# Performance work log

Measured on AMD Instinct MI355X. Metric: run time of the kernel, lower is better.

## Reference

```python
import jax, jax.numpy as jnp
import numpy as np

# --- Instant-NGP hash grid hyperparameters ---
L = 12            # n_levels (multires)
T = 2 ** 19       # hash table size per level
F = 2             # features per level -> feature_dim = L*F = 24
BASE_RES = 16
MAX_RES = 2048
N_PTS = 524288
D_OUT = 257

_growth = np.exp((np.log(MAX_RES) - np.log(BASE_RES)) / (L - 1))
RES = np.floor(BASE_RES * _growth ** np.arange(L)).astype(np.int32)  # per-level grid resolution
PRIMES = jnp.array([1, 2654435761, 805459861], dtype=jnp.uint32)
# 8 corner offsets of a voxel, [8,3] in {0,1}
OFFS = np.array([[(i >> 2) & 1, (i >> 1) & 1, i & 1] for i in range(8)], dtype=np.int32)
OFFS_U32 = jnp.asarray(OFFS, dtype=jnp.uint32)
OFFS_BOOL = jnp.asarray(OFFS.astype(bool))


def hash_encode(x, tables):
    """x: [N,3] in [0,1]; tables: [L,T,F]. Returns [N, L*F]."""
    outs = []
    for l in range(L):
        pos = x * RES[l]                      # [N,3]
        p0 = jnp.floor(pos)
        frac = pos - p0                       # [N,3] trilinear fractions
        corners = p0.astype(jnp.uint32)[:, None, :] + OFFS_U32[None]  # [N,8,3]
        h = corners * PRIMES[None, None, :]   # uint32 wrap-around mult
        idx = (h[..., 0] ^ h[..., 1] ^ h[..., 2]) & jnp.uint32(T - 1)  # [N,8]
        feats = tables[l][idx.astype(jnp.int32)]                       # [N,8,F] gather
        # trilinear weights: prod over dims of frac or (1-frac)
        w = jnp.prod(jnp.where(OFFS_BOOL[None], frac[:, None, :], 1.0 - frac[:, None, :]), axis=-1)  # [N,8]
        # windowed_embed: coarse-to-fine window weight; alpha = L (fully trained) -> weight 1.0
        outs.append(jnp.einsum('nc,ncf->nf', w, feats))
    return jnp.concatenate(outs, axis=-1)     # [N, L*F]


def setup_inputs() -> dict:
    key = jax.random.key(0)
    k1, k2, k3 = jax.random.split(key, 3)
    inputs = jax.random.uniform(k1, (N_PTS, 3), dtype=jnp.float32)
    tables = jax.random.normal(k2, (L, T, F), dtype=jnp.float32) * 1e-2
    W = jax.random.normal(k3, (L * F, D_OUT), dtype=jnp.float32) * (1.0 / np.sqrt(L * F))
    bias = jnp.zeros((D_OUT,), dtype=jnp.float32)
    return {"inputs": inputs, "tables": tables, "W": W, "bias": bias}


def reference(inputs, tables, W, bias):
    emb = hash_encode(inputs, tables)          # [N, 24]
    y = emb @ W + bias                         # TCNNLinear head, [N, 257]
    # torch.cat([x[:, :1], x[:, 1:]], -1) is identity; keep for fidelity
    return jnp.concatenate([y[:, :1], y[:, 1:]], axis=-1)
```

## Files before the change

### kernel.cpp

```cpp
#include <hip/hip_runtime.h>
#include <math.h>

#define NLEV 12
#define TSIZE (1u << 19)
#define TMASK (TSIZE - 1u)
#define DOUT 257
#define PPB 256
#define EMB 24
#define RSTRIDE 28
#define TP 128

struct ResArr { float r[NLEV]; };

__global__ __launch_bounds__(256)
void encode_kernel(const float* __restrict__ xin,
                   const float* __restrict__ tables,
                   float2* __restrict__ emb2,
                   int N, ResArr res)
{
    const int p = blockIdx.x * 256 + threadIdx.x;
    if (p >= N) return;
    const float px = xin[3 * p + 0];
    const float py = xin[3 * p + 1];
    const float pz = xin[3 * p + 2];
#pragma unroll 2
    for (int l = 0; l < NLEV; ++l) {
        const float rf = res.r[l];
        const float sx = px * rf, sy = py * rf, sz = pz * rf;
        const float gx = floorf(sx), gy = floorf(sy), gz = floorf(sz);
        const float tx = sx - gx, ty = sy - gy, tz = sz - gz;
        const unsigned ix = (unsigned)gx, iy = (unsigned)gy, iz = (unsigned)gz;
        const unsigned hx0 = ix,               hx1 = ix + 1u;
        const unsigned hy0 = iy * 2654435761u, hy1 = hy0 + 2654435761u;
        const unsigned hz0 = iz * 805459861u,  hz1 = hz0 + 805459861u;
        const float2* __restrict__ tab = (const float2*)tables + (size_t)l * TSIZE;
        float2 f0 = tab[(hx0 ^ hy0 ^ hz0) & TMASK];
        float2 f1 = tab[(hx0 ^ hy0 ^ hz1) & TMASK];
        float2 f2 = tab[(hx0 ^ hy1 ^ hz0) & TMASK];
        float2 f3 = tab[(hx0 ^ hy1 ^ hz1) & TMASK];
        float2 f4 = tab[(hx1 ^ hy0 ^ hz0) & TMASK];
        float2 f5 = tab[(hx1 ^ hy0 ^ hz1) & TMASK];
        float2 f6 = tab[(hx1 ^ hy1 ^ hz0) & TMASK];
        float2 f7 = tab[(hx1 ^ hy1 ^ hz1) & TMASK];
        const float u0 = 1.0f - tx, u1 = tx;
        const float v0 = 1.0f - ty, v1 = ty;
        const float s0 = 1.0f - tz, s1 = tz;
        const float w0 = (u0 * v0) * s0;
        const float w1 = (u0 * v0) * s1;
        const float w2 = (u0 * v1) * s0;
        const float w3 = (u0 * v1) * s1;
        const float w4 = (u1 * v0) * s0;
        const float w5 = (u1 * v0) * s1;
        const float w6 = (u1 * v1) * s0;
        const float w7 = (u1 * v1) * s1;
        float a = w0 * f0.x;
        float b = w0 * f0.y;
        a = fmaf(w1, f1.x, a);  b = fmaf(w1, f1.y, b);
        a = fmaf(w2, f2.x, a);  b = fmaf(w2, f2.y, b);
        a = fmaf(w3, f3.x, a);  b = fmaf(w3, f3.y, b);
        a = fmaf(w4, f4.x, a);  b = fmaf(w4, f4.y, b);
        a = fmaf(w5, f5.x, a);  b = fmaf(w5, f5.y, b);
        a = fmaf(w6, f6.x, a);  b = fmaf(w6, f6.y, b);
        a = fmaf(w7, f7.x, a);  b = fmaf(w7, f7.y, b);
        emb2[(size_t)l * N + p] = make_float2(a, b);
    }
}

__global__ __launch_bounds__(256)
void head_kernel(const float2* __restrict__ emb2,
                 const float* __restrict__ Wm,
                 const float* __restrict__ bias,
                 float* __restrict__ out,
                 int N)
{
    __shared__ float2 sm[NLEV][TP];
    const int tid  = threadIdx.x;
    const int base = blockIdx.x * TP;
    const int nv   = min(TP, N - base);

    float wcol[EMB];
#pragma unroll
    for (int k = 0; k < EMB; ++k) wcol[k] = Wm[k * DOUT + tid];
    const float bj = bias[tid];

#pragma unroll
    for (int i = 0; i < (NLEV * TP) / 256; ++i) {
        const int f = i * 256 + tid;
        const int l = f >> 7;
        const int n = f & (TP - 1);
        if (n < nv) sm[l][n] = emb2[(size_t)l * N + base + n];
    }
    __syncthreads();

    float* orow = out + (size_t)base * DOUT + tid;
    for (int n = 0; n < nv; ++n, orow += DOUT) {
        float accA = bj, accB = 0.0f;
#pragma unroll
        for (int l = 0; l < NLEV; l += 2) {
            const float2 q0 = sm[l][n];
            const float2 q1 = sm[l + 1][n];
            accA = fmaf(q0.x, wcol[2 * l + 0], accA);
            accB = fmaf(q0.y, wcol[2 * l + 1], accB);
            accA = fmaf(q1.x, wcol[2 * l + 2], accA);
            accB = fmaf(q1.y, wcol[2 * l + 3], accB);
        }
        *orow = accA + accB;
    }

    if (tid < nv) {
        float acc = bias[256];
#pragma unroll
        for (int l = 0; l < NLEV; ++l) {
            const float2 q = sm[l][tid];
            acc = fmaf(q.x, Wm[(2 * l) * DOUT + 256],
                  fmaf(q.y, Wm[(2 * l + 1) * DOUT + 256], acc));
        }
        out[(size_t)(base + tid) * DOUT + 256] = acc;
    }
}

__global__ __launch_bounds__(256)
void hashgrid_head_kernel(const float* __restrict__ xin,
                          const float* __restrict__ tables,
                          const float* __restrict__ Wm,
                          const float* __restrict__ bias,
                          float* __restrict__ out,
                          int N, ResArr res)
{
    __shared__ float emb[PPB * RSTRIDE];
    const int tid  = threadIdx.x;
    const int base = blockIdx.x * PPB;
    const int p    = base + tid;

    float wcol[EMB];
#pragma unroll
    for (int k = 0; k < EMB; ++k) wcol[k] = Wm[k * DOUT + tid];
    const float bj = bias[tid];

    const bool extra = (tid < 64);
    float wext[EMB];
    float bext = 0.0f;
    if (extra) {
#pragma unroll
        for (int k = 0; k < EMB; ++k) wext[k] = Wm[k * DOUT + 256];
        bext = bias[256];
    }

    if (p < N) {
        const float px = xin[3 * p + 0];
        const float py = xin[3 * p + 1];
        const float pz = xin[3 * p + 2];
#pragma unroll 2
        for (int l = 0; l < NLEV; ++l) {
            const float rf = res.r[l];
            const float sx = px * rf, sy = py * rf, sz = pz * rf;
            const float gx = floorf(sx), gy = floorf(sy), gz = floorf(sz);
            const float tx = sx - gx, ty = sy - gy, tz = sz - gz;
            const unsigned ix = (unsigned)gx, iy = (unsigned)gy, iz = (unsigned)gz;
            const unsigned hx0 = ix,               hx1 = ix + 1u;
            const unsigned hy0 = iy * 2654435761u, hy1 = hy0 + 2654435761u;
            const unsigned hz0 = iz * 805459861u,  hz1 = hz0 + 805459861u;
            const float2* __restrict__ tab = (const float2*)tables + (size_t)l * TSIZE;
            float2 f0 = tab[(hx0 ^ hy0 ^ hz0) & TMASK];
            float2 f1 = tab[(hx0 ^ hy0 ^ hz1) & TMASK];
            float2 f2 = tab[(hx0 ^ hy1 ^ hz0) & TMASK];
            float2 f3 = tab[(hx0 ^ hy1 ^ hz1) & TMASK];
            float2 f4 = tab[(hx1 ^ hy0 ^ hz0) & TMASK];
            float2 f5 = tab[(hx1 ^ hy0 ^ hz1) & TMASK];
            float2 f6 = tab[(hx1 ^ hy1 ^ hz0) & TMASK];
            float2 f7 = tab[(hx1 ^ hy1 ^ hz1) & TMASK];
            const float u0 = 1.0f - tx, u1 = tx;
            const float v0 = 1.0f - ty, v1 = ty;
            const float s0 = 1.0f - tz, s1 = tz;
            const float w0 = (u0 * v0) * s0;
            const float w1 = (u0 * v0) * s1;
            const float w2 = (u0 * v1) * s0;
            const float w3 = (u0 * v1) * s1;
            const float w4 = (u1 * v0) * s0;
            const float w5 = (u1 * v0) * s1;
            const float w6 = (u1 * v1) * s0;
            const float w7 = (u1 * v1) * s1;
            float a = w0 * f0.x;
            float b = w0 * f0.y;
            a = fmaf(w1, f1.x, a);  b = fmaf(w1, f1.y, b);
            a = fmaf(w2, f2.x, a);  b = fmaf(w2, f2.y, b);
            a = fmaf(w3, f3.x, a);  b = fmaf(w3, f3.y, b);
            a = fmaf(w4, f4.x, a);  b = fmaf(w4, f4.y, b);
            a = fmaf(w5, f5.x, a);  b = fmaf(w5, f5.y, b);
            a = fmaf(w6, f6.x, a);  b = fmaf(w6, f6.y, b);
            a = fmaf(w7, f7.x, a);  b = fmaf(w7, f7.y, b);
            *(float2*)&emb[tid * RSTRIDE + 2 * l] = make_float2(a, b);
        }
    }

    __syncthreads();

    const int nvalid = min(PPB, N - base);
    for (int n = 0; n < nvalid; ++n) {
        const float4* e4 = (const float4*)&emb[n * RSTRIDE];
        float4 q0 = e4[0], q1 = e4[1], q2 = e4[2], q3 = e4[3], q4 = e4[4], q5 = e4[5];
        float e[EMB] = {q0.x, q0.y, q0.z, q0.w, q1.x, q1.y, q1.z, q1.w,
                        q2.x, q2.y, q2.z, q2.w, q3.x, q3.y, q3.z, q3.w,
                        q4.x, q4.y, q4.z, q4.w, q5.x, q5.y, q5.z, q5.w};
        float acc = bj;
#pragma unroll
        for (int k = 0; k < EMB; ++k) acc = fmaf(e[k], wcol[k], acc);
        out[(size_t)(base + n) * DOUT + tid] = acc;
        if (extra) {
            float acc2 = bext;
#pragma unroll
            for (int k = 0; k < EMB; ++k) acc2 = fmaf(e[k], wext[k], acc2);
            if (tid == 0) out[(size_t)(base + n) * DOUT + 256] = acc2;
        }
    }
}

extern "C" void kernel_launch(void* const* d_in, const int* in_sizes, int n_in,
                              void* d_out, int out_size, void* d_ws, size_t ws_size,
                              hipStream_t stream) {
    const float* xin    = (const float*)d_in[0];
    const float* tables = (const float*)d_in[1];
    const float* Wm     = (const float*)d_in[2];
    const float* bias   = (const float*)d_in[3];
    float* out = (float*)d_out;
    const int N = in_sizes[0] / 3;

    ResArr res;
    const double growth = exp((log(2048.0) - log(16.0)) / 11.0);
    for (int l = 0; l < NLEV; ++l)
        res.r[l] = (float)floor(16.0 * pow(growth, (double)l));

    const size_t need = (size_t)NLEV * (size_t)N * sizeof(float2);
    if (d_ws != nullptr && ws_size >= need) {
        float2* emb2 = (float2*)d_ws;
        hipLaunchKernelGGL(encode_kernel, dim3((N + 255) / 256), dim3(256), 0, stream,
                           xin, tables, emb2, N, res);
        hipLaunchKernelGGL(head_kernel, dim3((N + TP - 1) / TP), dim3(256), 0, stream,
                           emb2, Wm, bias, out, N);
    } else {
        const int grid = (N + PPB - 1) / PPB;
        hipLaunchKernelGGL(hashgrid_head_kernel, dim3(grid), dim3(PPB), 0, stream,
                           xin, tables, Wm, bias, out, N, res);
    }
}
```

Baseline: 917.0 us.

## Split hash encoding across levels per block and read embeddings directly in head

The encode kernel now launches one block per (level, point-chunk), so level-major block ordering keeps each level's hash table hot in cache and gives more parallel work. The head kernel drops its shared-memory staging and __syncthreads, reading embedding values straight from global memory with uniform (broadcast) loads per point. This trades repeated point-coordinate loads and redundant per-thread global reads for less cache thrashing and no LDS staging.

```diff
diff --git a/kernel.cpp b/kernel.cpp
--- a/kernel.cpp
+++ b/kernel.cpp
@@ -16,54 +16,55 @@
 void encode_kernel(const float* __restrict__ xin,
                    const float* __restrict__ tables,
                    float2* __restrict__ emb2,
-                   int N, ResArr res)
+                   int N, int nbpl, ResArr res)
 {
-    const int p = blockIdx.x * 256 + threadIdx.x;
+    const int lvl = blockIdx.x / nbpl;
+    const int bx  = blockIdx.x - lvl * nbpl;
+    const int p   = bx * 256 + threadIdx.x;
     if (p >= N) return;
+
     const float px = xin[3 * p + 0];
     const float py = xin[3 * p + 1];
     const float pz = xin[3 * p + 2];
-#pragma unroll 2
-    for (int l = 0; l < NLEV; ++l) {
-        const float rf = res.r[l];
-        const float sx = px * rf, sy = py * rf, sz = pz * rf;
-        const float gx = floorf(sx), gy = floorf(sy), gz = floorf(sz);
-        const float tx = sx - gx, ty = sy - gy, tz = sz - gz;
-        const unsigned ix = (unsigned)gx, iy = (unsigned)gy, iz = (unsigned)gz;
-        const unsigned hx0 = ix,               hx1 = ix + 1u;
-        const unsigned hy0 = iy * 2654435761u, hy1 = hy0 + 2654435761u;
-        const unsigned hz0 = iz * 805459861u,  hz1 = hz0 + 805459861u;
-        const float2* __restrict__ tab = (const float2*)tables + (size_t)l * TSIZE;
-        float2 f0 = tab[(hx0 ^ hy0 ^ hz0) & TMASK];
-        float2 f1 = tab[(hx0 ^ hy0 ^ hz1) & TMASK];
-        float2 f2 = tab[(hx0 ^ hy1 ^ hz0) & TMASK];
-        float2 f3 = tab[(hx0 ^ hy1 ^ hz1) & TMASK];
-        float2 f4 = tab[(hx1 ^ hy0 ^ hz0) & TMASK];
-        float2 f5 = tab[(hx1 ^ hy0 ^ hz1) & TMASK];
-        float2 f6 = tab[(hx1 ^ hy1 ^ hz0) & TMASK];
-        float2 f7 = tab[(hx1 ^ hy1 ^ hz1) & TMASK];
-        const float u0 = 1.0f - tx, u1 = tx;
-        const float v0 = 1.0f - ty, v1 = ty;
-        const float s0 = 1.0f - tz, s1 = tz;
-        const float w0 = (u0 * v0) * s0;
-        const float w1 = (u0 * v0) * s1;
-        const float w2 = (u0 * v1) * s0;
-        const float w3 = (u0 * v1) * s1;
-        const float w4 = (u1 * v0) * s0;
-        const float w5 = (u1 * v0) * s1;
-        const float w6 = (u1 * v1) * s0;
-        const float w7 = (u1 * v1) * s1;
-        float a = w0 * f0.x;
-        float b = w0 * f0.y;
-        a = fmaf(w1, f1.x, a);  b = fmaf(w1, f1.y, b);
-        a = fmaf(w2, f2.x, a);  b = fmaf(w2, f2.y, b);
-        a = fmaf(w3, f3.x, a);  b = fmaf(w3, f3.y, b);
-        a = fmaf(w4, f4.x, a);  b = fmaf(w4, f4.y, b);
-        a = fmaf(w5, f5.x, a);  b = fmaf(w5, f5.y, b);
-        a = fmaf(w6, f6.x, a);  b = fmaf(w6, f6.y, b);
-        a = fmaf(w7, f7.x, a);  b = fmaf(w7, f7.y, b);
-        emb2[(size_t)l * N + p] = make_float2(a, b);
-    }
+
+    const float rf = res.r[lvl];
+    const float sx = px * rf, sy = py * rf, sz = pz * rf;
+    const float gx = floorf(sx), gy = floorf(sy), gz = floorf(sz);
+    const float tx = sx - gx, ty = sy - gy, tz = sz - gz;
+    const unsigned ix = (unsigned)gx, iy = (unsigned)gy, iz = (unsigned)gz;
+    const unsigned hx0 = ix,               hx1 = ix + 1u;
+    const unsigned hy0 = iy * 2654435761u, hy1 = hy0 + 2654435761u;
+    const unsigned hz0 = iz * 805459861u,  hz1 = hz0 + 805459861u;
+    const float2* __restrict__ tab = (const float2*)tables + (size_t)lvl * TSIZE;
+    float2 f0 = tab[(hx0 ^ hy0 ^ hz0) & TMASK];
+    float2 f1 = tab[(hx0 ^ hy0 ^ hz1) & TMASK];
+    float2 f2 = tab[(hx0 ^ hy1 ^ hz0) & TMASK];
+    float2 f3 = tab[(hx0 ^ hy1 ^ hz1) & TMASK];
+    float2 f4 = tab[(hx1 ^ hy0 ^ hz0) & TMASK];
+    float2 f5 = tab[(hx1 ^ hy0 ^ hz1) & TMASK];
+    float2 f6 = tab[(hx1 ^ hy1 ^ hz0) & TMASK];
+    float2 f7 = tab[(hx1 ^ hy1 ^ hz1) & TMASK];
+    const float u0 = 1.0f - tx, u1 = tx;
+    const float v0 = 1.0f - ty, v1 = ty;
+    const float s0 = 1.0f - tz, s1 = tz;
+    const float w0 = (u0 * v0) * s0;
+    const float w1 = (u0 * v0) * s1;
+    const float w2 = (u0 * v1) * s0;
+    const float w3 = (u0 * v1) * s1;
+    const float w4 = (u1 * v0) * s0;
+    const float w5 = (u1 * v0) * s1;
+    const float w6 = (u1 * v1) * s0;
+    const float w7 = (u1 * v1) * s1;
+    float a = w0 * f0.x;
+    float b = w0 * f0.y;
+    a = fmaf(w1, f1.x, a);  b = fmaf(w1, f1.y, b);
+    a = fmaf(w2, f2.x, a);  b = fmaf(w2, f2.y, b);
+    a = fmaf(w3, f3.x, a);  b = fmaf(w3, f3.y, b);
+    a = fmaf(w4, f4.x, a);  b = fmaf(w4, f4.y, b);
+    a = fmaf(w5, f5.x, a);  b = fmaf(w5, f5.y, b);
+    a = fmaf(w6, f6.x, a);  b = fmaf(w6, f6.y, b);
+    a = fmaf(w7, f7.x, a);  b = fmaf(w7, f7.y, b);
+    emb2[(size_t)lvl * N + p] = make_float2(a, b);
 }
 
 __global__ __launch_bounds__(256)
@@ -73,7 +74,6 @@
                  float* __restrict__ out,
                  int N)
 {
-    __shared__ float2 sm[NLEV][TP];
     const int tid  = threadIdx.x;
     const int base = blockIdx.x * TP;
     const int nv   = min(TP, N - base);
@@ -83,39 +83,29 @@
     for (int k = 0; k < EMB; ++k) wcol[k] = Wm[k * DOUT + tid];
     const float bj = bias[tid];
 
-#pragma unroll
-    for (int i = 0; i < (NLEV * TP) / 256; ++i) {
-        const int f = i * 256 + tid;
-        const int l = f >> 7;
-        const int n = f & (TP - 1);
-        if (n < nv) sm[l][n] = emb2[(size_t)l * N + base + n];
-    }
-    __syncthreads();
-
     float* orow = out + (size_t)base * DOUT + tid;
+#pragma unroll 2
     for (int n = 0; n < nv; ++n, orow += DOUT) {
         float accA = bj, accB = 0.0f;
 #pragma unroll
-        for (int l = 0; l < NLEV; l += 2) {
-            const float2 q0 = sm[l][n];
-            const float2 q1 = sm[l + 1][n];
-            accA = fmaf(q0.x, wcol[2 * l + 0], accA);
-            accB = fmaf(q0.y, wcol[2 * l + 1], accB);
-            accA = fmaf(q1.x, wcol[2 * l + 2], accA);
-            accB = fmaf(q1.y, wcol[2 * l + 3], accB);
+        for (int l = 0; l < NLEV; ++l) {
+            const float2 q = emb2[(size_t)l * N + base + n];
+            accA = fmaf(q.x, wcol[2 * l + 0], accA);
+            accB = fmaf(q.y, wcol[2 * l + 1], accB);
         }
         *orow = accA + accB;
     }
 
     if (tid < nv) {
+        const int p = base + tid;
         float acc = bias[256];
 #pragma unroll
         for (int l = 0; l < NLEV; ++l) {
-            const float2 q = sm[l][tid];
+            const float2 q = emb2[(size_t)l * N + p];
             acc = fmaf(q.x, Wm[(2 * l) * DOUT + 256],
                   fmaf(q.y, Wm[(2 * l + 1) * DOUT + 256], acc));
         }
-        out[(size_t)(base + tid) * DOUT + 256] = acc;
+        out[(size_t)p * DOUT + 256] = acc;
     }
 }
 
@@ -233,8 +223,9 @@
     const size_t need = (size_t)NLEV * (size_t)N * sizeof(float2);
     if (d_ws != nullptr && ws_size >= need) {
         float2* emb2 = (float2*)d_ws;
-        hipLaunchKernelGGL(encode_kernel, dim3((N + 255) / 256), dim3(256), 0, stream,
-                           xin, tables, emb2, N, res);
+        const int nbpl = (N + 255) / 256;
+        hipLaunchKernelGGL(encode_kernel, dim3(nbpl * NLEV), dim3(256), 0, stream,
+                           xin, tables, emb2, N, nbpl, res);
         hipLaunchKernelGGL(head_kernel, dim3((N + TP - 1) / TP), dim3(256), 0, stream,
                            emb2, Wm, bias, out, N);
     } else {
```

After: 1.440 ms. 1.57x slower.

## Split hash encoding across levels in the grid for per-level table locality

Applied to the files above, without the earlier changes.

The encode kernel now assigns each block to a single hash level, with each thread handling two points, instead of one thread walking all twelve levels. Blocks that run at the same time then gather from the same 4 MB level table, which should improve L2 hit rates, and two independent gather sets per thread add memory-level parallelism. The cost is that point coordinates are reloaded once per level, and the fused fallback kernel is only refactored through a shared helper.

```diff
diff --git a/kernel.cpp b/kernel.cpp
--- a/kernel.cpp
+++ b/kernel.cpp
@@ -9,60 +9,98 @@
 #define EMB 24
 #define RSTRIDE 28
 #define TP 128
+#define EPT 2
+#define EPB (256 * EPT)
 
 struct ResArr { float r[NLEV]; };
+
+struct Corner { unsigned idx[8]; float w[8]; };
+
+__device__ __forceinline__ void hash_corners(float rf, float px, float py, float pz,
+                                             Corner& c)
+{
+    const float sx = px * rf, sy = py * rf, sz = pz * rf;
+    const float gx = floorf(sx), gy = floorf(sy), gz = floorf(sz);
+    const float tx = sx - gx, ty = sy - gy, tz = sz - gz;
+    const unsigned ix = (unsigned)gx, iy = (unsigned)gy, iz = (unsigned)gz;
+    const unsigned hx0 = ix,               hx1 = ix + 1u;
+    const unsigned hy0 = iy * 2654435761u, hy1 = hy0 + 2654435761u;
+    const unsigned hz0 = iz * 805459861u,  hz1 = hz0 + 805459861u;
+    c.idx[0] = (hx0 ^ hy0 ^ hz0) & TMASK;
+    c.idx[1] = (hx0 ^ hy0 ^ hz1) & TMASK;
+    c.idx[2] = (hx0 ^ hy1 ^ hz0) & TMASK;
+    c.idx[3] = (hx0 ^ hy1 ^ hz1) & TMASK;
+    c.idx[4] = (hx1 ^ hy0 ^ hz0) & TMASK;
+    c.idx[5] = (hx1 ^ hy0 ^ hz1) & TMASK;
+    c.idx[6] = (hx1 ^ hy1 ^ hz0) & TMASK;
+    c.idx[7] = (hx1 ^ hy1 ^ hz1) & TMASK;
+    const float u0 = 1.0f - tx, u1 = tx;
+    const float v0 = 1.0f - ty, v1 = ty;
+    const float s0 = 1.0f - tz, s1 = tz;
+    c.w[0] = (u0 * v0) * s0;
+    c.w[1] = (u0 * v0) * s1;
+    c.w[2] = (u0 * v1) * s0;
+    c.w[3] = (u0 * v1) * s1;
+    c.w[4] = (u1 * v0) * s0;
+    c.w[5] = (u1 * v0) * s1;
+    c.w[6] = (u1 * v1) * s0;
+    c.w[7] = (u1 * v1) * s1;
+}
 
 __global__ __launch_bounds__(256)
 void encode_kernel(const float* __restrict__ xin,
                    const float* __restrict__ tables,
                    float2* __restrict__ emb2,
-                   int N, ResArr res)
-{
-    const int p = blockIdx.x * 256 + threadIdx.x;
-    if (p >= N) return;
-    const float px = xin[3 * p + 0];
-    const float py = xin[3 * p + 1];
-    const float pz = xin[3 * p + 2];
-#pragma unroll 2
-    for (int l = 0; l < NLEV; ++l) {
-        const float rf = res.r[l];
-        const float sx = px * rf, sy = py * rf, sz = pz * rf;
-        const float gx = floorf(sx), gy = floorf(sy), gz = floorf(sz);
-        const float tx = sx - gx, ty = sy - gy, tz = sz - gz;
-        const unsigned ix = (unsigned)gx, iy = (unsigned)gy, iz = (unsigned)gz;
-        const unsigned hx0 = ix,               hx1 = ix + 1u;
-        const unsigned hy0 = iy * 2654435761u, hy1 = hy0 + 2654435761u;
-        const unsigned hz0 = iz * 805459861u,  hz1 = hz0 + 805459861u;
-        const float2* __restrict__ tab = (const float2*)tables + (size_t)l * TSIZE;
-        float2 f0 = tab[(hx0 ^ hy0 ^ hz0) & TMASK];
-        float2 f1 = tab[(hx0 ^ hy0 ^ hz1) & TMASK];
-        float2 f2 = tab[(hx0 ^ hy1 ^ hz0) & TMASK];
-        float2 f3 = tab[(hx0 ^ hy1 ^ hz1) & TMASK];
-        float2 f4 = tab[(hx1 ^ hy0 ^ hz0) & TMASK];
-        float2 f5 = tab[(hx1 ^ hy0 ^ hz1) & TMASK];
-        float2 f6 = tab[(hx1 ^ hy1 ^ hz0) & TMASK];
-        float2 f7 = tab[(hx1 ^ hy1 ^ hz1) & TMASK];
-        const float u0 = 1.0f - tx, u1 = tx;
-        const float v0 = 1.0f - ty, v1 = ty;
-        const float s0 = 1.0f - tz, s1 = tz;
-        const float w0 = (u0 * v0) * s0;
-        const float w1 = (u0 * v0) * s1;
-        const float w2 = (u0 * v1) * s0;
-        const float w3 = (u0 * v1) * s1;
-        const float w4 = (u1 * v0) * s0;
-        const float w5 = (u1 * v0) * s1;
-        const float w6 = (u1 * v1) * s0;
-        const float w7 = (u1 * v1) * s1;
-        float a = w0 * f0.x;
-        float b = w0 * f0.y;
-        a = fmaf(w1, f1.x, a);  b = fmaf(w1, f1.y, b);
-        a = fmaf(w2, f2.x, a);  b = fmaf(w2, f2.y, b);
-        a = fmaf(w3, f3.x, a);  b = fmaf(w3, f3.y, b);
-        a = fmaf(w4, f4.x, a);  b = fmaf(w4, f4.y, b);
-        a = fmaf(w5, f5.x, a);  b = fmaf(w5, f5.y, b);
-        a = fmaf(w6, f6.x, a);  b = fmaf(w6, f6.y, b);
-        a = fmaf(w7, f7.x, a);  b = fmaf(w7, f7.y, b);
-        emb2[(size_t)l * N + p] = make_float2(a, b);
+                   int N, int nbpl, ResArr res)
+{
+    const int lvl = blockIdx.x / nbpl;
+    const int bx  = blockIdx.x - lvl * nbpl;
+    const int pA  = bx * EPB + threadIdx.x;
+    const int pB  = pA + 256;
+    if (pA >= N) return;
+    const bool hasB = (pB < N);
+
+    const float ax = xin[3 * pA + 0];
+    const float ay = xin[3 * pA + 1];
+    const float az = xin[3 * pA + 2];
+    float bx_ = 0.f, by_ = 0.f, bz_ = 0.f;
+    if (hasB) {
+        bx_ = xin[3 * pB + 0];
+        by_ = xin[3 * pB + 1];
+        bz_ = xin[3 * pB + 2];
+    }
+
+    const float rf = res.r[lvl];
+    Corner cA, cB;
+    hash_corners(rf, ax, ay, az, cA);
+    hash_corners(rf, bx_, by_, bz_, cB);
+
+    const float2* __restrict__ tab = (const float2*)tables + (size_t)lvl * TSIZE;
+
+    float2 fA[8], fB[8];
+#pragma unroll
+    for (int i = 0; i < 8; ++i) fA[i] = tab[cA.idx[i]];
+#pragma unroll
+    for (int i = 0; i < 8; ++i) fB[i] = tab[cB.idx[i]];
+
+    float a = cA.w[0] * fA[0].x;
+    float b = cA.w[0] * fA[0].y;
+#pragma unroll
+    for (int i = 1; i < 8; ++i) {
+        a = fmaf(cA.w[i], fA[i].x, a);
+        b = fmaf(cA.w[i], fA[i].y, b);
+    }
+    emb2[(size_t)lvl * N + pA] = make_float2(a, b);
+
+    if (hasB) {
+        float a2 = cB.w[0] * fB[0].x;
+        float b2 = cB.w[0] * fB[0].y;
+#pragma unroll
+        for (int i = 1; i < 8; ++i) {
+            a2 = fmaf(cB.w[i], fB[i].x, a2);
+            b2 = fmaf(cB.w[i], fB[i].y, b2);
+        }
+        emb2[(size_t)lvl * N + pB] = make_float2(a2, b2);
     }
 }
 
@@ -153,42 +191,19 @@
 #pragma unroll 2
         for (int l = 0; l < NLEV; ++l) {
             const float rf = res.r[l];
-            const float sx = px * rf, sy = py * rf, sz = pz * rf;
-            const float gx = floorf(sx), gy = floorf(sy), gz = floorf(sz);
-            const float tx = sx - gx, ty = sy - gy, tz = sz - gz;
-            const unsigned ix = (unsigned)gx, iy = (unsigned)gy, iz = (unsigned)gz;
-            const unsigned hx0 = ix,               hx1 = ix + 1u;
-            const unsigned hy0 = iy * 2654435761u, hy1 = hy0 + 2654435761u;
-            const unsigned hz0 = iz * 805459861u,  hz1 = hz0 + 805459861u;
+            Corner c;
+            hash_corners(rf, px, py, pz, c);
             const float2* __restrict__ tab = (const float2*)tables + (size_t)l * TSIZE;
-            float2 f0 = tab[(hx0 ^ hy0 ^ hz0) & TMASK];
-            float2 f1 = tab[(hx0 ^ hy0 ^ hz1) & TMASK];
-            float2 f2 = tab[(hx0 ^ hy1 ^ hz0) & TMASK];
-            float2 f3 = tab[(hx0 ^ hy1 ^ hz1) & TMASK];
-            float2 f4 = tab[(hx1 ^ hy0 ^ hz0) & TMASK];
-            float2 f5 = tab[(hx1 ^ hy0 ^ hz1) & TMASK];
-            float2 f6 = tab[(hx1 ^ hy1 ^ hz0) & TMASK];
-            float2 f7 = tab[(hx1 ^ hy1 ^ hz1) & TMASK];
-            const float u0 = 1.0f - tx, u1 = tx;
-            const float v0 = 1.0f - ty, v1 = ty;
-            const float s0 = 1.0f - tz, s1 = tz;
-            const float w0 = (u0 * v0) * s0;
-            const float w1 = (u0 * v0) * s1;
-            const float w2 = (u0 * v1) * s0;
-            const float w3 = (u0 * v1) * s1;
-            const float w4 = (u1 * v0) * s0;
-            const float w5 = (u1 * v0) * s1;
-            const float w6 = (u1 * v1) * s0;
-            const float w7 = (u1 * v1) * s1;
-            float a = w0 * f0.x;
-            float b = w0 * f0.y;
-            a = fmaf(w1, f1.x, a);  b = fmaf(w1, f1.y, b);
-            a = fmaf(w2, f2.x, a);  b = fmaf(w2, f2.y, b);
-            a = fmaf(w3, f3.x, a);  b = fmaf(w3, f3.y, b);
-            a = fmaf(w4, f4.x, a);  b = fmaf(w4, f4.y, b);
-            a = fmaf(w5, f5.x, a);  b = fmaf(w5, f5.y, b);
-            a = fmaf(w6, f6.x, a);  b = fmaf(w6, f6.y, b);
-            a = fmaf(w7, f7.x, a);  b = fmaf(w7, f7.y, b);
+            float2 f[8];
+#pragma unroll
+            for (int i = 0; i < 8; ++i) f[i] = tab[c.idx[i]];
+            float a = c.w[0] * f[0].x;
+            float b = c.w[0] * f[0].y;
+#pragma unroll
+            for (int i = 1; i < 8; ++i) {
+                a = fmaf(c.w[i], f[i].x, a);
+                b = fmaf(c.w[i], f[i].y, b);
+            }
             *(float2*)&emb[tid * RSTRIDE + 2 * l] = make_float2(a, b);
         }
     }
@@ -233,8 +248,9 @@
     const size_t need = (size_t)NLEV * (size_t)N * sizeof(float2);
     if (d_ws != nullptr && ws_size >= need) {
         float2* emb2 = (float2*)d_ws;
-        hipLaunchKernelGGL(encode_kernel, dim3((N + 255) / 256), dim3(256), 0, stream,
-                           xin, tables, emb2, N, res);
+        const int nbpl = (N + EPB - 1) / EPB;
+        hipLaunchKernelGGL(encode_kernel, dim3(nbpl * NLEV), dim3(256), 0, stream,
+                           xin, tables, emb2, N, nbpl, res);
         hipLaunchKernelGGL(head_kernel, dim3((N + TP - 1) / TP), dim3(256), 0, stream,
                            emb2, Wm, bias, out, N);
     } else {
```

Result: faster. 821.6 us (-10.4%).
